# Performance work log

Measured on AMD Instinct MI355X. Metric: run time of the kernel, lower is better.

Reference implementation:

```python
import jax, jax.numpy as jnp
import numpy as np

# Model constants (match init_kwargs)
H, P, N, G, NL, K = 32, 64, 128, 1, 15, 4   # heads, head_dim, state, groups, lambda levels, conv width
HID, T, BATCH = 1024, 1024, 1
INTER = H * P                    # 2048
CONV_DIM = INTER + 2 * G * N     # 2304
PROJ = INTER + CONV_DIM + H * (NL + 1)  # 4864
EPS = 1e-5


def _level_matrix(t_len: int) -> np.ndarray:
    """Fenwick-tree level assignment: for query t, prefix [0,t] splits into
    power-of-two segments from binary expansion of t+1; segment of length 2^l -> level l."""
    lm = np.zeros((t_len, t_len), dtype=np.int32)
    for t in range(t_len):
        n = t + 1
        while n > 0:
            lb = n & (-n)
            lm[t, n - lb:n] = lb.bit_length() - 1
            n -= lb
    return lm


def setup_inputs() -> dict:
    key = jax.random.key(0)
    ks = jax.random.split(key, 4)
    return {
        "hidden_states": jax.random.normal(ks[0], (BATCH, T, HID), jnp.float32),
        "in_proj_w": jax.random.normal(ks[1], (PROJ, HID), jnp.float32) / np.sqrt(HID).astype(np.float32),
        "in_proj_b": jnp.zeros((PROJ,), jnp.float32),
        "conv_w": jax.random.normal(ks[2], (CONV_DIM, K), jnp.float32) / np.sqrt(K).astype(np.float32),
        "dt_bias": jnp.ones((H,), jnp.float32),
        "A_log": jnp.log(jnp.arange(1, H + 1, dtype=jnp.float32)),
        "L_param": jnp.ones((H, NL), jnp.float32),
        "D": jnp.ones((H,), jnp.float32),
        "rmsnorm_w": jnp.ones((INTER,), jnp.float32),
        "out_proj_w": jax.random.normal(ks[3], (HID, INTER), jnp.float32) / np.sqrt(INTER).astype(np.float32),
        "out_proj_b": jnp.zeros((HID,), jnp.float32),
        "level_mat": jnp.asarray(_level_matrix(T)),  # (T,T) int32, data-independent
    }


def reference(hidden_states, in_proj_w, in_proj_b, conv_w, dt_bias, A_log,
              L_param, D, rmsnorm_w, out_proj_w, out_proj_b, level_mat):
    b, t, _ = hidden_states.shape
    # in_proj and split: [z | xBC | dt | dl]
    zxbcdtdl = hidden_states @ in_proj_w.T + in_proj_b
    z, xBC, dt, dl = jnp.split(zxbcdtdl, [INTER, INTER + CONV_DIM, INTER + CONV_DIM + H], axis=-1)
    # depthwise causal conv1d (width K) + SiLU
    xp = jnp.pad(xBC, ((0, 0), (K - 1, 0), (0, 0)))
    conv = sum(xp[:, w:w + t, :] * conv_w[:, w] for w in range(K))
    xBC = jax.nn.silu(conv)
    x, Bm, Cm = jnp.split(xBC, [INTER, INTER + G * N], axis=-1)
    x = x.reshape(b, t, H, P)          # v pre-scale
    Bm = Bm.reshape(b, t, G, N)        # keys
    Cm = Cm.reshape(b, t, G, N)        # queries
    dl = dl.reshape(b, t, H, NL)
    # D residual uses unscaled x (matches hmamba_chunk_scan_combined ordering)
    D_res = x * D[None, None, :, None]
    dt = jax.nn.softplus(dt + dt_bias)            # (b,t,H)
    v = x * dt[..., None]                          # (b,t,H,P)
    A = -jnp.exp(A_log)                            # (H,)
    g = A * dt                                     # (b,t,H), per-token log-decay (<=0)
    Ls = jax.nn.softplus(L_param * dl)             # (b,t,H,NL) per-token level scales
    # cumulative log-decay; decay(t,s) = exp(cg_t - cg_s), s<=t
    cg = jnp.cumsum(g, axis=1).transpose(0, 2, 1)  # (b,H,t)
    mask = jnp.tril(jnp.ones((t, t), bool))
    logdecay = jnp.where(mask, cg[:, :, :, None] - cg[:, :, None, :], -jnp.inf)
    decay = jnp.exp(logdecay)                      # (b,H,t,s)
    # hierarchical level scale H[t,s] = Ls[b,t,h, level(t,s)]
    Hmat = jnp.take_along_axis(Ls.transpose(0, 2, 1, 3), level_mat[None, None, :, :], axis=-1)  # (b,H,t,s)
    scores = jnp.einsum('btgn,bsgn->bgts', Cm, Bm)  # (b,G,t,s), G=1 broadcasts over heads
    att = scores * decay * Hmat                     # (b,H,t,s), masked via decay=0
    y = jnp.einsum('bhts,bshp->bthp', att, v) + D_res
    y = y.reshape(b, t, INTER)
    # gated RMSNorm with norm_before_gate=False: normalize(y * silu(z)) * w
    yg = y * jax.nn.silu(z)
    y = yg * jax.lax.rsqrt(jnp.mean(yg * yg, axis=-1, keepdims=True) + EPS) * rmsnorm_w
    return y @ out_proj_w.T + out_proj_b
```

## Files before the change

kernel.cpp:

```cpp
#include <hip/hip_runtime.h>
#include <hip/hip_bf16.h>
#include <math.h>

#define T_LEN 1024
#define HID 1024
#define NHEAD 32
#define HDIM 64
#define NSTATE 128
#define NLVL 15
#define KCONV 4
#define INTER 2048
#define CONV_DIM 2304
#define PROJ 4864
#define NPROJ16 4352
#define NPROJF 512
#define EPS 1e-5f

typedef __attribute__((ext_vector_type(8))) _Float16 half8;
typedef __attribute__((ext_vector_type(4))) float float4v;
typedef unsigned short ushort_t;

__device__ __forceinline__ float softplus_f(float x) {
  return fmaxf(x, 0.f) + log1pf(expf(-fabsf(x)));
}
__device__ __forceinline__ float silu_f(float x) {
  return x / (1.f + expf(-x));
}
__device__ __forceinline__ ushort_t f2h(float f) {
  union { _Float16 h; ushort_t u; } v;
  v.h = (_Float16)f;
  return v.u;
}
__device__ __forceinline__ float h2f(ushort_t u) {
  union { ushort_t u; _Float16 h; } v;
  v.u = u;
  return (float)v.h;
}
__device__ __forceinline__ void gload_lds16(const void* g, void* l) {
  __builtin_amdgcn_global_load_lds(
      (const __attribute__((address_space(1))) void*)g,
      (__attribute__((address_space(3))) void*)l, 16, 0, 0);
}

#define N4_HS  (T_LEN * HID / 4)
#define N4_WI  (PROJ * HID / 4)
#define N4_WO  (HID * INTER / 4)
__global__ __launch_bounds__(256) void prep_f16(
    const float* __restrict__ hs, const float* __restrict__ wi,
    const float* __restrict__ wo, ushort_t* __restrict__ hsb,
    ushort_t* __restrict__ wib, ushort_t* __restrict__ wob) {
  int i = blockIdx.x * 256 + threadIdx.x;
  const float* src; ushort_t* dst; int j;
  if (i < N4_HS)              { src = hs; dst = hsb; j = i; }
  else if (i < N4_HS + N4_WI) { src = wi; dst = wib; j = i - N4_HS; }
  else                        { src = wo; dst = wob; j = i - N4_HS - N4_WI; }
  float4 v = reinterpret_cast<const float4*>(src)[j];
  union { ushort_t u[4]; unsigned long long ll; } o;
  o.u[0] = f2h(v.x); o.u[1] = f2h(v.y); o.u[2] = f2h(v.z); o.u[3] = f2h(v.w);
  reinterpret_cast<unsigned long long*>(dst)[j] = o.ll;
}

__global__ __launch_bounds__(256) void gemm_in(
    const ushort_t* __restrict__ A, const ushort_t* __restrict__ B,
    const float* __restrict__ bias,
    ushort_t* __restrict__ Ch, float* __restrict__ Cf) {
  const int K = HID;
  __shared__ ushort_t As[2][128][64];
  __shared__ ushort_t Bs[2][128][64];
  const int tid = threadIdx.x;
  const int w = tid >> 6, L = tid & 63;
  const int lid = blockIdx.y * 38 + blockIdx.x;
  const int J = (lid & 7) * 38 + (lid >> 3);
  const int n0 = (J >> 3) * 128, m0 = (J & 7) * 128;
  const int mq = (w & 1) * 64, nq = (w >> 1) * 64;
  const int srow = L >> 3;
  const int swst = ((L & 7) ^ srow) * 8;

  float4v acc[4][4];
#pragma unroll
  for (int i = 0; i < 4; ++i)
#pragma unroll
    for (int j = 0; j < 4; ++j) acc[i][j] = (float4v){0.f, 0.f, 0.f, 0.f};

  const int niter = K / 64;
  {
#pragma unroll
    for (int j = 0; j < 4; ++j) {
      int r0 = 8 * (w * 4 + j);
      gload_lds16(A + (size_t)(m0 + r0 + srow) * K + swst, &As[0][r0][0]);
      gload_lds16(B + (size_t)(n0 + r0 + srow) * K + swst, &Bs[0][r0][0]);
    }
  }
  for (int it = 0; it < niter; ++it) {
    __syncthreads();
    if (it + 1 < niter) {
      const int kk = (it + 1) * 64;
      const int nb = (it + 1) & 1;
#pragma unroll
      for (int j = 0; j < 4; ++j) {
        int r0 = 8 * (w * 4 + j);
        gload_lds16(A + (size_t)(m0 + r0 + srow) * K + kk + swst, &As[nb][r0][0]);
        gload_lds16(B + (size_t)(n0 + r0 + srow) * K + kk + swst, &Bs[nb][r0][0]);
      }
    }
    const int cb = it & 1;
    half8 af[4][2], bf[4][2];
#pragma unroll
    for (int kk2 = 0; kk2 < 2; ++kk2) {
      const int sw = ((kk2 * 4 + (L >> 4)) ^ (L & 7)) * 8;
#pragma unroll
      for (int t = 0; t < 4; ++t) {
        af[t][kk2] = *reinterpret_cast<const half8*>(&As[cb][mq + t * 16 + (L & 15)][sw]);
        bf[t][kk2] = *reinterpret_cast<const half8*>(&Bs[cb][nq + t * 16 + (L & 15)][sw]);
      }
    }
#pragma unroll
    for (int kk2 = 0; kk2 < 2; ++kk2)
#pragma unroll
      for (int mt = 0; mt < 4; ++mt)
#pragma unroll
        for (int nt = 0; nt < 4; ++nt)
          acc[mt][nt] = __builtin_amdgcn_mfma_f32_16x16x32_f16(af[mt][kk2], bf[nt][kk2],
                                                               acc[mt][nt], 0, 0, 0);
  }
  const int qrow = (L >> 4) * 4;
  const bool tof16 = (n0 < NPROJ16);
#pragma unroll
  for (int mt = 0; mt < 4; ++mt) {
#pragma unroll
    for (int nt = 0; nt < 4; ++nt) {
      int col = n0 + nq + nt * 16 + (L & 15);
      float bv = bias[col];
#pragma unroll
      for (int r = 0; r < 4; ++r) {
        int row = m0 + mq + mt * 16 + qrow + r;
        float v = acc[mt][nt][r] + bv;
        if (tof16) Ch[(size_t)row * NPROJ16 + col] = f2h(v);
        else       Cf[(size_t)row * NPROJF + (col - NPROJ16)] = v;
      }
    }
  }
}

__global__ __launch_bounds__(256) void gemm_f16_sk(
    const ushort_t* __restrict__ A, const ushort_t* __restrict__ B,
    float* __restrict__ Cpart, int M, int N, int K, int Kc) {
  __shared__ ushort_t As[2][128][64];
  __shared__ ushort_t Bs[2][128][64];
  const int tid = threadIdx.x;
  const int w = tid >> 6, L = tid & 63;
  const int d = (blockIdx.z * 8 + blockIdx.y) * 8 + blockIdx.x;
  const int J = (d & 7) * 32 + (d >> 3);
  const int kz = J >> 6;
  const int n0 = ((J >> 3) & 7) * 128, m0 = (J & 7) * 128;
  const int kbeg = kz * Kc;
  float* __restrict__ C = Cpart + (size_t)kz * M * N;
  const int mq = (w & 1) * 64, nq = (w >> 1) * 64;
  const int srow = L >> 3;
  const int swst = ((L & 7) ^ srow) * 8;

  float4v acc[4][4];
#pragma unroll
  for (int i = 0; i < 4; ++i)
#pragma unroll
    for (int j = 0; j < 4; ++j) acc[i][j] = (float4v){0.f, 0.f, 0.f, 0.f};

  const int niter = Kc / 64;
  {
#pragma unroll
    for (int j = 0; j < 4; ++j) {
      int r0 = 8 * (w * 4 + j);
      gload_lds16(A + (size_t)(m0 + r0 + srow) * K + kbeg + swst, &As[0][r0][0]);
      gload_lds16(B + (size_t)(n0 + r0 + srow) * K + kbeg + swst, &Bs[0][r0][0]);
    }
  }
  for (int it = 0; it < niter; ++it) {
    __syncthreads();
    if (it + 1 < niter) {
      const int kk = kbeg + (it + 1) * 64;
      const int nb = (it + 1) & 1;
#pragma unroll
      for (int j = 0; j < 4; ++j) {
        int r0 = 8 * (w * 4 + j);
        gload_lds16(A + (size_t)(m0 + r0 + srow) * K + kk + swst, &As[nb][r0][0]);
        gload_lds16(B + (size_t)(n0 + r0 + srow) * K + kk + swst, &Bs[nb][r0][0]);
      }
    }
    const int cb = it & 1;
    half8 af[4][2], bf[4][2];
#pragma unroll
    for (int kk2 = 0; kk2 < 2; ++kk2) {
      const int sw = ((kk2 * 4 + (L >> 4)) ^ (L & 7)) * 8;
#pragma unroll
      for (int t = 0; t < 4; ++t) {
        af[t][kk2] = *reinterpret_cast<const half8*>(&As[cb][mq + t * 16 + (L & 15)][sw]);
        bf[t][kk2] = *reinterpret_cast<const half8*>(&Bs[cb][nq + t * 16 + (L & 15)][sw]);
      }
    }
#pragma unroll
    for (int kk2 = 0; kk2 < 2; ++kk2)
#pragma unroll
      for (int mt = 0; mt < 4; ++mt)
#pragma unroll
        for (int nt = 0; nt < 4; ++nt)
          acc[mt][nt] = __builtin_amdgcn_mfma_f32_16x16x32_f16(af[mt][kk2], bf[nt][kk2],
                                                               acc[mt][nt], 0, 0, 0);
  }
  const int qrow = (L >> 4) * 4;
#pragma unroll
  for (int mt = 0; mt < 4; ++mt) {
#pragma unroll
    for (int nt = 0; nt < 4; ++nt) {
      int col = n0 + nq + nt * 16 + (L & 15);
#pragma unroll
      for (int r = 0; r < 4; ++r) {
        int row = m0 + mq + mt * 16 + qrow + r;
        C[(size_t)row * N + col] = acc[mt][nt][r];
      }
    }
  }
}

__global__ __launch_bounds__(256) void reduce_out4(const float* __restrict__ p,
                                                   const float* __restrict__ bias,
                                                   float* __restrict__ out, int MN) {
  int i = blockIdx.x * 256 + threadIdx.x;
  if (i * 4 >= MN) return;
  float4 a = reinterpret_cast<const float4*>(p)[i];
  float4 b = reinterpret_cast<const float4*>(p + MN)[i];
  float4 c = reinterpret_cast<const float4*>(p + 2 * (size_t)MN)[i];
  float4 d = reinterpret_cast<const float4*>(p + 3 * (size_t)MN)[i];
  int col = (i * 4) & (HID - 1);
  float4 bv = *reinterpret_cast<const float4*>(bias + col);
  float4 o;
  o.x = a.x + b.x + c.x + d.x + bv.x;
  o.y = a.y + b.y + c.y + d.y + bv.y;
  o.z = a.z + b.z + c.z + d.z + bv.z;
  o.w = a.w + b.w + c.w + d.w + bv.w;
  reinterpret_cast<float4*>(out)[i] = o;
}

__global__ __launch_bounds__(64) void scan_g(
    const float* __restrict__ zxf, const float* __restrict__ dt_bias,
    const float* __restrict__ A_log, float* __restrict__ dtbuf,
    double* __restrict__ cgd) {
  const int h = blockIdx.x, l = threadIdx.x;
  const float bh = dt_bias[h];
  const float ah = -expf(A_log[h]);
  double pre[16];
  double acc = 0.0;
#pragma unroll
  for (int i = 0; i < 16; ++i) {
    int t = l * 16 + i;
    float dt = softplus_f(zxf[(size_t)t * NPROJF + h] + bh);
    dtbuf[t * NHEAD + h] = dt;
    acc += (double)(ah * dt);
    pre[i] = acc;
  }
  double s = acc;
#pragma unroll
  for (int off = 1; off < 64; off <<= 1) {
    double o = __shfl_up(s, off, 64);
    if (l >= off) s += o;
  }
  const double base = s - acc;
  double* cr = cgd + (size_t)h * T_LEN + l * 16;
#pragma unroll
  for (int i = 0; i < 16; ++i) cr[i] = base + pre[i];
}

__global__ __launch_bounds__(256) void conv_fused(
    const ushort_t* __restrict__ zxh, const float* __restrict__ conv_w,
    const float* __restrict__ dtbuf, const float* __restrict__ Dp,
    ushort_t* __restrict__ vt, float* __restrict__ ybuf,
    ushort_t* __restrict__ Bb, ushort_t* __restrict__ Cb) {
  __shared__ ushort_t Vl[64][68];
  __shared__ float dtl[64];
  const int tq = blockIdx.x, cy = blockIdx.y;
  const int t0 = tq * 64;
  const int tid = threadIdx.x;
  const int lane = tid & 63, g = tid >> 6;
  const bool vpath = (cy < 32);
  const int ccol = vpath ? cy * 64 + lane : INTER + (cy - 32) * 64 + lane;
  const int zcol = INTER + ccol;
  float cw[KCONV];
#pragma unroll
  for (int w = 0; w < KCONV; ++w) cw[w] = conv_w[ccol * KCONV + w];
  if (vpath && tid < 64) dtl[tid] = dtbuf[(t0 + tid) * NHEAD + cy];
  const float Dh = vpath ? Dp[cy] : 0.f;

  float xv[19];
#pragma unroll
  for (int i = 0; i < 19; ++i) {
    int tt = t0 + g * 16 - 3 + i;
    if (tt >= 0) {
      xv[i] = h2f(zxh[(size_t)tt * NPROJ16 + zcol]);
    } else xv[i] = 0.f;
  }
  __syncthreads();
#pragma unroll
  for (int i = 0; i < 16; ++i) {
    float acc = xv[i] * cw[0] + xv[i + 1] * cw[1] + xv[i + 2] * cw[2] + xv[i + 3] * cw[3];
    float sil = silu_f(acc);
    int tl = g * 16 + i;
    int t = t0 + tl;
    if (vpath) {
      ushort_t vh = f2h(sil * dtl[tl]);
      Vl[tl][lane] = vh;
      ybuf[(size_t)t * INTER + cy * 64 + lane] = sil * Dh;
    } else if (ccol < INTER + NSTATE) {
      Bb[t * NSTATE + (ccol - INTER)] = f2h(sil);
    } else {
      Cb[t * NSTATE + (ccol - INTER - NSTATE)] = f2h(sil);
    }
  }
  if (vpath) {
    __syncthreads();
#pragma unroll
    for (int rep = 0; rep < 2; ++rep) {
      int u = tid + 256 * rep;
      int p = u >> 3, t8 = (u & 7) * 8;
      union { ushort_t u16[8]; half8 h; } o;
#pragma unroll
      for (int j = 0; j < 8; ++j) o.u16[j] = Vl[t8 + j][p];
      *reinterpret_cast<half8*>(vt + (size_t)(cy * 64 + p) * T_LEN + t0 + t8) = o.h;
    }
  }
}

__global__ __launch_bounds__(256) void qk_gemm(
    const ushort_t* __restrict__ Cq, const ushort_t* __restrict__ Bk,
    ushort_t* __restrict__ S) {
  const int idx = blockIdx.x;
  int qt = (int)(0.5f * (sqrtf(8.f * (float)idx + 1.f) - 1.f));
  if ((qt + 1) * (qt + 2) / 2 <= idx) ++qt;
  if (qt * (qt + 1) / 2 > idx) --qt;
  const int st = idx - qt * (qt + 1) / 2;
  const int tid = threadIdx.x, w = tid >> 6, L = tid & 63;
  const int q0 = qt * 64 + (w & 1) * 32;
  const int s0 = st * 64 + (w >> 1) * 32;

  half8 af[2][4], bf[2][4];
#pragma unroll
  for (int mt = 0; mt < 2; ++mt)
#pragma unroll
    for (int ks = 0; ks < 4; ++ks) {
      af[mt][ks] = *reinterpret_cast<const half8*>(
          Cq + (size_t)(q0 + mt * 16 + (L & 15)) * NSTATE + ks * 32 + (L >> 4) * 8);
      bf[mt][ks] = *reinterpret_cast<const half8*>(
          Bk + (size_t)(s0 + mt * 16 + (L & 15)) * NSTATE + ks * 32 + (L >> 4) * 8);
    }
  float4v acc[2][2];
#pragma unroll
  for (int i = 0; i < 2; ++i)
#pragma unroll
    for (int j = 0; j < 2; ++j) acc[i][j] = (float4v){0.f, 0.f, 0.f, 0.f};
#pragma unroll
  for (int ks = 0; ks < 4; ++ks)
#pragma unroll
    for (int mt = 0; mt < 2; ++mt)
#pragma unroll
      for (int nt = 0; nt < 2; ++nt)
        acc[mt][nt] = __builtin_amdgcn_mfma_f32_16x16x32_f16(af[mt][ks], bf[nt][ks],
                                                             acc[mt][nt], 0, 0, 0);
  const int qrow = (L >> 4) * 4;
#pragma unroll
  for (int mt = 0; mt < 2; ++mt)
#pragma unroll
    for (int nt = 0; nt < 2; ++nt) {
      int col = s0 + nt * 16 + (L & 15);
#pragma unroll
      for (int r = 0; r < 4; ++r)
        S[(size_t)(q0 + mt * 16 + qrow + r) * T_LEN + col] = f2h(acc[mt][nt][r]);
    }
}

__global__ __launch_bounds__(256) void attn_mfma(
    const ushort_t* __restrict__ S, const ushort_t* __restrict__ vt,
    const double* __restrict__ cgd, const float* __restrict__ zxf,
    const float* __restrict__ L_param, float* __restrict__ ybuf) {
  __shared__ ushort_t Vtl[64][72];
  __shared__ float Lsl[64][17];
  __shared__ __align__(16) float cgq[64];
  __shared__ __align__(16) float cgs[64];

  const int item = blockIdx.x;
  const int h = item / 40;
  const int rem = item - h * 40;
  int qt, j;
  if (rem < 4)        { qt = rem;                 j = 0; }
  else if (rem < 12)  { qt = 4 + (rem - 4) / 2;   j = (rem - 4) % 2; }
  else if (rem < 24)  { qt = 8 + (rem - 12) / 3;  j = (rem - 12) % 3; }
  else                { qt = 12 + (rem - 24) / 4; j = (rem - 24) % 4; }

  const int tid = threadIdx.x;
  const int w = tid >> 6, L = tid & 63;
  const int tq0 = qt * 64;
  const double* cgh = cgd + (size_t)h * T_LEN;
  const double base = cgh[tq0];

  for (int i = tid; i < 64 * NLVL; i += 256) {
    int r = i / NLVL, l = i - r * NLVL;
    float lp = L_param[h * NLVL + l];
    float dl = zxf[(size_t)(tq0 + r) * NPROJF + NHEAD + h * NLVL + l];
    Lsl[r][l] = softplus_f(lp * dl);
  }
  if (tid < 64) cgq[tid] = (float)(cgh[tq0 + tid] - base);

  float4v yac[4];
#pragma unroll
  for (int i = 0; i < 4; ++i) yac[i] = (float4v){0.f, 0.f, 0.f, 0.f};

  const int qloc = w * 16 + (L & 15);
  const int tg = tq0 + qloc;
  const int qrow = w * 16 + ((L >> 4) << 2);

  const int st0 = 4 * j;
  const int st1 = min(4 * j + 4, qt + 1);
  for (int st = st0; st < st1; ++st) {
    const int ts0 = st * 64;
    __syncthreads();
    half8 sv0 = *reinterpret_cast<const half8*>(
        S + (size_t)tg * T_LEN + ts0 + (L >> 4) * 8);
    half8 sv1 = *reinterpret_cast<const half8*>(
        S + (size_t)tg * T_LEN + ts0 + 32 + (L >> 4) * 8);
#pragma unroll
    for (int i = 0; i < 2; ++i) {
      int u = tid + 256 * i;
      int p = u >> 3, sc = (u & 7) * 8;
      *reinterpret_cast<half8*>(&Vtl[p][sc]) =
          *reinterpret_cast<const half8*>(vt + (size_t)(h * HDIM + p) * T_LEN + ts0 + sc);
    }
    if (tid < 64) cgs[tid] = (float)(cgh[ts0 + tid] - base);
    __syncthreads();

    const float cq = cgq[qloc];
    half8 af[2];
#pragma unroll
    for (int ks = 0; ks < 2; ++ks) {
      const half8 sv = ks ? sv1 : sv0;
      const int sb = ks * 32 + (L >> 4) * 8;
      float4 c0 = *reinterpret_cast<const float4*>(&cgs[sb]);
      float4 c1 = *reinterpret_cast<const float4*>(&cgs[sb + 4]);
      float csv[8] = {c0.x, c0.y, c0.z, c0.w, c1.x, c1.y, c1.z, c1.w};
      union { ushort_t u[8]; half8 h; } o;
#pragma unroll
      for (int jj = 0; jj < 8; ++jj) {
        int sg = ts0 + sb + jj;
        float val = 0.f;
        if (sg <= tg) {
          int lvl = 31 - __clz((unsigned)(sg ^ (tg + 1)));
          val = (float)sv[jj] * __expf(cq - csv[jj]) * Lsl[qloc][lvl];
        }
        o.u[jj] = f2h(val);
      }
      af[ks] = o.h;
    }
#pragma unroll
    for (int ks = 0; ks < 2; ++ks) {
#pragma unroll
      for (int pt = 0; pt < 4; ++pt) {
        half8 bfv = *reinterpret_cast<const half8*>(&Vtl[pt * 16 + (L & 15)][ks * 32 + (L >> 4) * 8]);
        yac[pt] = __builtin_amdgcn_mfma_f32_16x16x32_f16(af[ks], bfv, yac[pt], 0, 0, 0);
      }
    }
  }
#pragma unroll
  for (int pt = 0; pt < 4; ++pt) {
    int p = pt * 16 + (L & 15);
#pragma unroll
    for (int r = 0; r < 4; ++r) {
      int q = qrow + r;
      atomicAdd(ybuf + (size_t)(tq0 + q) * INTER + h * HDIM + p, yac[pt][r]);
    }
  }
}

__global__ __launch_bounds__(256) void rmsnorm_gate(
    const float* __restrict__ ybuf, const ushort_t* __restrict__ zxh,
    const float* __restrict__ w, ushort_t* __restrict__ yhf) {
  __shared__ float red[4];
  const int t = blockIdx.x, tid = threadIdx.x;
  const size_t ro = (size_t)t * NPROJ16;
  const float* yrow = ybuf + (size_t)t * INTER;
  float yg[8];
  float ss = 0.f;
#pragma unroll
  for (int i = 0; i < 8; ++i) {
    int c = tid + 256 * i;
    float z = h2f(zxh[ro + c]);
    float g = yrow[c] * silu_f(z);
    yg[i] = g;
    ss += g * g;
  }
#pragma unroll
  for (int off = 32; off; off >>= 1) ss += __shfl_down(ss, off, 64);
  if ((tid & 63) == 0) red[tid >> 6] = ss;
  __syncthreads();
  if (tid == 0) red[0] = red[0] + red[1] + red[2] + red[3];
  __syncthreads();
  const float scale = rsqrtf(red[0] / (float)INTER + EPS);
#pragma unroll
  for (int i = 0; i < 8; ++i) {
    int c = tid + 256 * i;
    yhf[(size_t)t * INTER + c] = f2h(yg[i] * scale * w[c]);
  }
}

extern "C" void kernel_launch(void* const* d_in, const int* in_sizes, int n_in,
                              void* d_out, int out_size, void* d_ws, size_t ws_size,
                              hipStream_t stream) {
  const float* hs        = (const float*)d_in[0];
  const float* in_proj_w = (const float*)d_in[1];
  const float* in_proj_b = (const float*)d_in[2];
  const float* conv_w    = (const float*)d_in[3];
  const float* dt_bias   = (const float*)d_in[4];
  const float* A_log     = (const float*)d_in[5];
  const float* L_param   = (const float*)d_in[6];
  const float* Dp        = (const float*)d_in[7];
  const float* rms_w     = (const float*)d_in[8];
  const float* out_proj_w= (const float*)d_in[9];
  const float* out_proj_b= (const float*)d_in[10];
  float* out = (float*)d_out;

  char* W = (char*)d_ws;
  size_t off = 0;
  auto alloc = [&](size_t bytes) { void* p = W + off; off = (off + bytes + 255) & ~(size_t)255; return p; };
  double*   cgd = (double*)  alloc((size_t)NHEAD * T_LEN * 8);
  float*    zxf = (float*)   alloc((size_t)T_LEN * NPROJF * 4);
  float*    opp = (float*)   alloc((size_t)4 * T_LEN * HID * 4);
  float*    ybuf= (float*)   alloc((size_t)T_LEN * INTER * 4);
  float*    dtb = (float*)   alloc((size_t)T_LEN * NHEAD * 4);
  ushort_t* zxh = (ushort_t*)alloc((size_t)T_LEN * NPROJ16 * 2);
  ushort_t* hsb = (ushort_t*)alloc((size_t)T_LEN * HID * 2);
  ushort_t* Wib = (ushort_t*)alloc((size_t)PROJ * HID * 2);
  ushort_t* Wob = (ushort_t*)alloc((size_t)HID * INTER * 2);
  ushort_t* yhf = (ushort_t*)alloc((size_t)T_LEN * INTER * 2);
  ushort_t* vt  = (ushort_t*)alloc((size_t)T_LEN * INTER * 2);
  ushort_t* Bb  = (ushort_t*)alloc((size_t)T_LEN * NSTATE * 2);
  ushort_t* Cb  = (ushort_t*)alloc((size_t)T_LEN * NSTATE * 2);
  ushort_t* Sbuf= (ushort_t*)alloc((size_t)T_LEN * T_LEN * 2);

  prep_f16<<<(N4_HS + N4_WI + N4_WO) / 256, 256, 0, stream>>>(
      hs, in_proj_w, out_proj_w, hsb, Wib, Wob);

  gemm_in<<<dim3(PROJ / 128, T_LEN / 128), 256, 0, stream>>>(
      hsb, Wib, in_proj_b, zxh, zxf);

  scan_g<<<NHEAD, 64, 0, stream>>>(zxf, dt_bias, A_log, dtb, cgd);

  conv_fused<<<dim3(T_LEN / 64, 36), 256, 0, stream>>>(
      zxh, conv_w, dtb, Dp, vt, ybuf, Bb, Cb);

  qk_gemm<<<136, 256, 0, stream>>>(Cb, Bb, Sbuf);

  attn_mfma<<<NHEAD * 40, 256, 0, stream>>>(Sbuf, vt, cgd, zxf, L_param, ybuf);

  rmsnorm_gate<<<T_LEN, 256, 0, stream>>>(ybuf, zxh, rms_w, yhf);

  gemm_f16_sk<<<dim3(HID / 128, T_LEN / 128, 4), 256, 0, stream>>>(
      yhf, Wob, opp, T_LEN, HID, INTER, INTER / 4);
  reduce_out4<<<(T_LEN * HID / 4 + 255) / 256, 256, 0, stream>>>(
      opp, out_proj_b, out, T_LEN * HID);
}
```

Measured before the change: 194.9 us.

## Drop GEMM block swizzle and split off unmasked off-diagonal attention tiles

The two GEMM kernels drop their remapped block-index swizzle and use plain blockIdx tile coordinates. The attention inner loop now has a fast path for key tiles strictly below the diagonal, skipping the per-element causal check. The diagonal tile keeps the masked path. Removing the swizzle may lower L2 locality across neighbouring workgroups, and the launch grid dimensions must match the new direct mapping.

```diff
diff --git a/kernel.cpp b/kernel.cpp
--- a/kernel.cpp
+++ b/kernel.cpp
@@ -69,9 +69,7 @@
   __shared__ ushort_t Bs[2][128][64];
   const int tid = threadIdx.x;
   const int w = tid >> 6, L = tid & 63;
-  const int lid = blockIdx.y * 38 + blockIdx.x;
-  const int J = (lid & 7) * 38 + (lid >> 3);
-  const int n0 = (J >> 3) * 128, m0 = (J & 7) * 128;
+  const int n0 = blockIdx.x * 128, m0 = blockIdx.y * 128;
   const int mq = (w & 1) * 64, nq = (w >> 1) * 64;
   const int srow = L >> 3;
   const int swst = ((L & 7) ^ srow) * 8;
@@ -149,12 +147,9 @@
   __shared__ ushort_t Bs[2][128][64];
   const int tid = threadIdx.x;
   const int w = tid >> 6, L = tid & 63;
-  const int d = (blockIdx.z * 8 + blockIdx.y) * 8 + blockIdx.x;
-  const int J = (d & 7) * 32 + (d >> 3);
-  const int kz = J >> 6;
-  const int n0 = ((J >> 3) & 7) * 128, m0 = (J & 7) * 128;
-  const int kbeg = kz * Kc;
-  float* __restrict__ C = Cpart + (size_t)kz * M * N;
+  const int n0 = blockIdx.x * 128, m0 = blockIdx.y * 128;
+  const int kbeg = blockIdx.z * Kc;
+  float* __restrict__ C = Cpart + (size_t)blockIdx.z * M * N;
   const int mq = (w & 1) * 64, nq = (w >> 1) * 64;
   const int srow = L >> 3;
   const int swst = ((L & 7) ^ srow) * 8;
@@ -436,25 +431,44 @@
 
     const float cq = cgq[qloc];
     half8 af[2];
-#pragma unroll
-    for (int ks = 0; ks < 2; ++ks) {
-      const half8 sv = ks ? sv1 : sv0;
-      const int sb = ks * 32 + (L >> 4) * 8;
-      float4 c0 = *reinterpret_cast<const float4*>(&cgs[sb]);
-      float4 c1 = *reinterpret_cast<const float4*>(&cgs[sb + 4]);
-      float csv[8] = {c0.x, c0.y, c0.z, c0.w, c1.x, c1.y, c1.z, c1.w};
-      union { ushort_t u[8]; half8 h; } o;
-#pragma unroll
-      for (int jj = 0; jj < 8; ++jj) {
-        int sg = ts0 + sb + jj;
-        float val = 0.f;
-        if (sg <= tg) {
+    if (st < qt) {
+#pragma unroll
+      for (int ks = 0; ks < 2; ++ks) {
+        const half8 sv = ks ? sv1 : sv0;
+        const int sb = ks * 32 + (L >> 4) * 8;
+        float4 c0 = *reinterpret_cast<const float4*>(&cgs[sb]);
+        float4 c1 = *reinterpret_cast<const float4*>(&cgs[sb + 4]);
+        float csv[8] = {c0.x, c0.y, c0.z, c0.w, c1.x, c1.y, c1.z, c1.w};
+        union { ushort_t u[8]; half8 h; } o;
+#pragma unroll
+        for (int jj = 0; jj < 8; ++jj) {
+          int sg = ts0 + sb + jj;
           int lvl = 31 - __clz((unsigned)(sg ^ (tg + 1)));
-          val = (float)sv[jj] * __expf(cq - csv[jj]) * Lsl[qloc][lvl];
+          o.u[jj] = f2h((float)sv[jj] * __expf(cq - csv[jj]) * Lsl[qloc][lvl]);
         }
-        o.u[jj] = f2h(val);
-      }
-      af[ks] = o.h;
+        af[ks] = o.h;
+      }
+    } else {
+#pragma unroll
+      for (int ks = 0; ks < 2; ++ks) {
+        const half8 sv = ks ? sv1 : sv0;
+        const int sb = ks * 32 + (L >> 4) * 8;
+        float4 c0 = *reinterpret_cast<const float4*>(&cgs[sb]);
+        float4 c1 = *reinterpret_cast<const float4*>(&cgs[sb + 4]);
+        float csv[8] = {c0.x, c0.y, c0.z, c0.w, c1.x, c1.y, c1.z, c1.w};
+        union { ushort_t u[8]; half8 h; } o;
+#pragma unroll
+        for (int jj = 0; jj < 8; ++jj) {
+          int sg = ts0 + sb + jj;
+          float val = 0.f;
+          if (sg <= tg) {
+            int lvl = 31 - __clz((unsigned)(sg ^ (tg + 1)));
+            val = (float)sv[jj] * __expf(cq - csv[jj]) * Lsl[qloc][lvl];
+          }
+          o.u[jj] = f2h(val);
+        }
+        af[ks] = o.h;
+      }
     }
 #pragma unroll
     for (int ks = 0; ks < 2; ++ks) {
```

After: 195.4 us. Within noise of the previous version (+0.3%).
